# Performance work log

Hardware: AMD Instinct MI355X
Metric: run time of the kernel (lower is better)

Reference implementation:

```python
import jax, jax.numpy as jnp
import numpy as np

B, N, E = 16, 512, 131072
FEAT, EMB, H = 3, 512, 3
K1, K2 = 410, 205  # ceil(0.8*512), ceil(0.5*410) per PyG TopKPooling
NEG_SLOPE, EPS = 0.2, 1e-5


def _gat_conv(x, W, att_s, att_d, bias, src, tgt, valid, num_nodes):
    # PyG GATConv (concat=True): per-edge attention with segment softmax over targets.
    Hh, C = att_s.shape
    xp = (x @ W).reshape(-1, Hh, C)                      # [Nn,H,C]
    a_s = jnp.einsum('nhc,hc->nh', xp, att_s)
    a_d = jnp.einsum('nhc,hc->nh', xp, att_d)
    srcc = jnp.where(valid, src, 0)
    tgtc = jnp.where(valid, tgt, 0)
    e = jax.nn.leaky_relu(a_s[srcc] + a_d[tgtc], NEG_SLOPE)  # [Ee,H]
    seg = jnp.where(valid, tgt, num_nodes)               # invalid edges -> dummy segment
    emax = jax.ops.segment_max(e, seg, num_segments=num_nodes + 1)
    emax = jnp.where(jnp.isfinite(emax), emax, 0.0)
    ex = jnp.exp(e - emax[seg]) * valid[:, None].astype(e.dtype)
    den = jax.ops.segment_sum(ex, seg, num_segments=num_nodes + 1)
    alpha = ex / jnp.maximum(den[seg], 1e-16)            # [Ee,H]
    out = jax.ops.segment_sum(alpha[:, :, None] * xp[srcc], seg,
                              num_segments=num_nodes + 1)[:num_nodes]
    return out.reshape(num_nodes, Hh * C) + bias


def _bn(x, g, b):
    # BatchNorm1d, training-mode batch statistics (biased var), eps=1e-5
    m = x.mean(0)
    v = x.var(0)
    return (x - m) * jax.lax.rsqrt(v + EPS) * g + b


def _topk_pool(x, p, nb, n_per, k):
    # PyG TopKPooling: score = tanh(x.w/||w||), keep top-k per graph, scale by score
    score = jnp.tanh((x @ p) / jnp.linalg.norm(p))       # [nb*n_per]
    top_s, top_i = jax.lax.top_k(score.reshape(nb, n_per), k)
    perm = (top_i + jnp.arange(nb)[:, None] * n_per).reshape(-1)
    x_new = x[perm] * top_s.reshape(-1, 1)
    mapping = jnp.full((nb * n_per,), -1, jnp.int32).at[perm].set(
        jnp.arange(nb * k, dtype=jnp.int32))
    return x_new, mapping


def _pool_cat(x, nb, k):
    # [global_max_pool, global_mean_pool] over equal-size graphs
    xr = x.reshape(nb, k, -1)
    return jnp.concatenate([xr.max(1), xr.mean(1)], axis=1)


def _forward(x, W1, as1, ad1, bc1, Wh1, bh1, g1, be1, p1,
             W2, as2, ad2, bc2, Wh2, bh2, g2, be2, p2,
             Wl1, bl1, Wl2, bl2, edge_index):
    Nn = B * N
    src0, tgt0 = edge_index[0], edge_index[1]
    sl = jnp.arange(Nn, dtype=jnp.int32)                 # GATConv add_self_loops=True
    src1 = jnp.concatenate([src0, sl]); tgt1 = jnp.concatenate([tgt0, sl])
    valid1 = jnp.ones(src1.shape, bool)
    h = _gat_conv(x, W1, as1, ad1, bc1, src1, tgt1, valid1, Nn)
    h = jax.nn.relu(h @ Wh1 + bh1)
    h = _bn(h, g1, be1)
    h, mapping = _topk_pool(h, p1, B, N, K1)
    x1 = _pool_cat(h, B, K1)                             # [B, 2*EMB]
    # relabel edges to pooled node ids; drop edges with removed endpoints via mask
    s2 = mapping[src0]; t2 = mapping[tgt0]
    v2 = (s2 >= 0) & (t2 >= 0)
    sl2 = jnp.arange(B * K1, dtype=jnp.int32)
    src2 = jnp.concatenate([s2, sl2]); tgt2 = jnp.concatenate([t2, sl2])
    valid2 = jnp.concatenate([v2, jnp.ones(sl2.shape, bool)])
    h = _gat_conv(h, W2, as2, ad2, bc2, src2, tgt2, valid2, B * K1)
    h = jax.nn.relu(h @ Wh2 + bh2)
    h = _bn(h, g2, be2)
    h, _ = _topk_pool(h, p2, B, K1, K2)
    x2 = _pool_cat(h, B, K2)
    xg = x1 + x2
    xg = jax.nn.relu(xg @ Wl1 + bl1)                     # dropout p=0.5 disabled (eval)
    return xg @ Wl2 + bl2                                # [B, 256]


def setup_inputs() -> dict:
    key = jax.random.key(0)
    ks = jax.random.split(key, 16)
    x = jax.random.normal(ks[0], (B * N, FEAT), jnp.float32)
    goff = jnp.repeat(jnp.arange(B, dtype=jnp.int32), E // B) * N
    src = jax.random.randint(ks[1], (E,), 0, N, jnp.int32) + goff
    tgt = jax.random.randint(ks[2], (E,), 0, N, jnp.int32) + goff
    edge_index = jnp.stack([src, tgt])
    s = 0.05
    p = {
        'W1': jax.random.normal(ks[3], (FEAT, H * EMB)) * s,
        'as1': jax.random.normal(ks[4], (H, EMB)) * s,
        'ad1': jax.random.normal(ks[5], (H, EMB)) * s,
        'bc1': jnp.zeros((H * EMB,)),
        'Wh1': jax.random.normal(ks[6], (H * EMB, EMB)) * s,
        'bh1': jnp.zeros((EMB,)),
        'g1': jnp.ones((EMB,)), 'be1': jnp.zeros((EMB,)),
        'p1': jax.random.normal(ks[7], (EMB,)) * s,
        'W2': jax.random.normal(ks[8], (EMB, H * EMB)) * s,
        'as2': jax.random.normal(ks[9], (H, EMB)) * s,
        'ad2': jax.random.normal(ks[10], (H, EMB)) * s,
        'bc2': jnp.zeros((H * EMB,)),
        'Wh2': jax.random.normal(ks[11], (H * EMB, EMB)) * s,
        'bh2': jnp.zeros((EMB,)),
        'g2': jnp.ones((EMB,)), 'be2': jnp.zeros((EMB,)),
        'p2': jax.random.normal(ks[12], (EMB,)) * s,
        'Wl1': jax.random.normal(ks[13], (2 * EMB, 512)) * s,
        'bl1': jnp.zeros((512,)),
        'Wl2': jax.random.normal(ks[14], (512, 256)) * s,
        'bl2': jnp.zeros((256,)),
    }
    return {'x': x, 'edge_index': edge_index, **p}


def reference(x, edge_index, W1, as1, ad1, bc1, Wh1, bh1, g1, be1, p1,
              W2, as2, ad2, bc2, Wh2, bh2, g2, be2, p2, Wl1, bl1, Wl2, bl2):
    return _forward(x, W1, as1, ad1, bc1, Wh1, bh1, g1, be1, p1,
                    W2, as2, ad2, bc2, Wh2, bh2, g2, be2, p2,
                    Wl1, bl1, Wl2, bl2, edge_index)
```

## Files before the change

### kernel.cpp

```cpp
#include <hip/hip_runtime.h>
#include <hip/hip_bf16.h>
#include <math.h>

#define E_EDGES 131072
#define NN1 8192
#define NN2 6560
#define NG 16
#define NP1 512
#define KP1 410
#define KP2 205
#define F1 1536
#define EMB 512
#define MAXDEG 256

typedef __hip_bfloat16 bf16;
typedef __attribute__((ext_vector_type(8))) short short8;
typedef __attribute__((ext_vector_type(4))) float f32x4;
typedef __attribute__((ext_vector_type(4))) unsigned short us4;

__device__ inline float wred64(float v){
  #pragma unroll
  for (int o = 32; o; o >>= 1) v += __shfl_down(v, o);
  return v;
}
__device__ inline float b2f_raw(unsigned short u){
  return __uint_as_float((unsigned)u << 16);
}
union BFU { bf16 b; unsigned short u; };
__device__ inline unsigned short f2u(float v){ BFU x; x.b = __float2bfloat16(v); return x.u; }

__device__ __forceinline__ void gld16(const void* g, void* l){
  __builtin_amdgcn_global_load_lds(
      (const __attribute__((address_space(1))) void*)g,
      (__attribute__((address_space(3))) void*)l, 16, 0, 0);
}

__device__ inline void split_store(float v, bf16* __restrict__ ph, bf16* __restrict__ pl){
  bf16 hi = __float2bfloat16(v);
  *ph = hi;
  *pl = __float2bfloat16(v - __bfloat162float(hi));
}

__device__ inline void bn_from_acc(const float* __restrict__ bnacc, int c, float fM,
                                   float& mean, float& inv){
  mean = bnacc[c] / fM;
  float var = fmaxf(bnacc[512+c]/fM - mean*mean, 0.f);
  inv = 1.f / sqrtf(var + 1e-5f);
}

__global__ __launch_bounds__(256) void k_pre(
    const float* __restrict__ W1, const float* __restrict__ as1, const float* __restrict__ ad1,
    const float* __restrict__ Wh1, const float* __restrict__ bc1, const float* __restrict__ bh1,
    const float* __restrict__ W2, const float* __restrict__ as2, const float* __restrict__ ad2,
    const float* __restrict__ Wh2, const float* __restrict__ bc2, const float* __restrict__ bh2,
    float* __restrict__ was1, float* __restrict__ wad1, float* __restrict__ M1p,
    float* __restrict__ cvp,
    float* __restrict__ was2, float* __restrict__ wad2,
    float* __restrict__ Zb, int* __restrict__ cnt2, int* __restrict__ map,
    bf16* __restrict__ Th, bf16* __restrict__ Tl){
  int b = blockIdx.x, t = threadIdx.x;
  if (b < 24){
    int h = b / 8, rem = b % 8, jh = rem >> 2, kc = rem & 3;
    int j = jh*256 + t, c0 = kc*128;
    __shared__ float w1s[3][128];
    for (int i = t; i < 384; i += 256)
      w1s[i>>7][i&127] = W1[(i>>7)*1536 + h*512 + c0 + (i&127)];
    __syncthreads();
    const float* whc = Wh1 + (size_t)(h*512 + c0)*512 + j;
    float a0=0.f, a1=0.f, a2=0.f;
    #pragma unroll 8
    for (int c = 0; c < 128; c++){
      float v = whc[(size_t)c*512];
      a0 += w1s[0][c]*v; a1 += w1s[1][c]*v; a2 += w1s[2][c]*v;
    }
    float* dst = M1p + (size_t)kc*4608;
    dst[(h*3+0)*512 + j] = a0;
    dst[(h*3+1)*512 + j] = a1;
    dst[(h*3+2)*512 + j] = a2;
  } else if (b < 56){
    int b2 = b - 24;
    int which = b2 >> 4, rem = b2 & 15, jh = rem >> 3, kc = rem & 7;
    const float* bc = which ? bc2 : bc1;
    const float* Wh = which ? Wh2 : Wh1;
    const float* bh = which ? bh2 : bh1;
    int j = jh*256 + t, i0 = kc*192;
    float acc = (kc == 0) ? bh[j] : 0.f;
    #pragma unroll 8
    for (int i = 0; i < 192; i++)
      acc += bc[i0+i] * Wh[(size_t)(i0+i)*512 + j];
    cvp[(size_t)(which*8 + kc)*512 + j] = acc;
  } else if (b < 152){
    int b3 = b - 56;
    int y = b3 >> 4, et = b3 & 15;
    int kind = y / 3, h = y % 3;
    int w = t >> 6, lane = t & 63;
    const float* att = kind ? ad2 : as2;
    float a[8];
    #pragma unroll
    for (int u = 0; u < 8; u++) a[u] = att[h*512 + lane*8 + u];
    for (int r = w; r < 32; r += 4){
      int e = et*32 + r;
      const float4* row = (const float4*)(W2 + (size_t)e*1536 + h*512) + lane*2;
      float4 v0 = row[0], v1 = row[1];
      float d = v0.x*a[0]+v0.y*a[1]+v0.z*a[2]+v0.w*a[3]
              + v1.x*a[4]+v1.y*a[5]+v1.z*a[6]+v1.w*a[7];
      d = wred64(d);
      if (lane == 0) (kind ? wad2 : was2)[h*512 + e] = d;
    }
  } else if (b < 170){
    if (t < 64){
      int bb = b - 152;
      int kind = bb / 9, r = bb % 9, h = r / 3, f = r % 3;
      const float* att = kind ? ad1 : as1;
      float s = 0.f;
      for (int c = t; c < 512; c += 64) s += W1[f*1536 + h*512 + c] * att[h*512 + c];
      s = wred64(s);
      if (t == 0) (kind ? wad1 : was1)[h*3 + f] = s;
    }
  } else if (b < 236){
    int i = (b - 170)*256 + t;
    if (i < 2048){ Zb[i] = 0.f; }
    else if (i < 2048 + NN2){ cnt2[i - 2048] = 1; }
    else if (i < 2048 + NN2 + NN1){ map[i - 2048 - NN2] = -1; }
  } else {
    int bb = b - 236;
    int z = bb % 3; int rr = bb / 3; int by = rr >> 3, bx = rr & 7;
    const float* A = W2 + (size_t)z*512;
    const float* B = Wh2 + (size_t)z*512*512;
    __shared__ __align__(16) short sAh[4096], sAl[4096], sBh[4096], sBl[4096];
    int w = t >> 6, lane = t & 63;
    int l16 = lane & 15, q = lane >> 4;
    int bm = by*64, bn = bx*64;
    int am  = t >> 2, akw = (t & 3)*16;
    int bnl = t & 63, bkq = (t >> 6)*16;
    f32x4 acc[4];
    #pragma unroll
    for (int nf = 0; nf < 4; nf++) acc[nf] = (f32x4){0.f,0.f,0.f,0.f};
    float va[16], vb[16];
    #define GS_LOAD(K0) do { \
      _Pragma("unroll") for (int u = 0; u < 4; u++){ \
        float4 v4 = *(const float4*)(A + (size_t)(bm+am)*1536 + (K0) + akw + u*4); \
        va[u*4]=v4.x; va[u*4+1]=v4.y; va[u*4+2]=v4.z; va[u*4+3]=v4.w; } \
      _Pragma("unroll") for (int u = 0; u < 16; u++) \
        vb[u] = B[(size_t)((K0) + bkq + u)*512 + bn + bnl]; \
    } while(0)
    GS_LOAD(0);
    for (int it = 0; it < 8; it++){
      #pragma unroll
      for (int hh = 0; hh < 2; hh++){
        short8 ah_, al_, bh_, bl_;
        #pragma unroll
        for (int jj = 0; jj < 8; jj++){
          float v = va[hh*8+jj];
          unsigned short hu = f2u(v);
          ah_[jj] = (short)hu; al_[jj] = (short)f2u(v - b2f_raw(hu));
          v = vb[hh*8+jj];
          hu = f2u(v);
          bh_[jj] = (short)hu; bl_[jj] = (short)f2u(v - b2f_raw(hu));
        }
        int aoff = am*64  + ((((akw>>3) + hh) ^ (am  & 7)) << 3);
        *(short8*)(sAh + aoff) = ah_;
        *(short8*)(sAl + aoff) = al_;
        int boff = bnl*64 + ((((bkq>>3) + hh) ^ (bnl & 7)) << 3);
        *(short8*)(sBh + boff) = bh_;
        *(short8*)(sBl + boff) = bl_;
      }
      __syncthreads();
      if (it < 7) GS_LOAD((it+1)*64);
      #pragma unroll
      for (int ks = 0; ks < 2; ks++){
        int gc = ks*4 + q;
        int ar = w*16 + l16;
        int ao = ar*64 + ((gc ^ (ar & 7)) << 3);
        short8 afh = *(const short8*)(sAh + ao);
        short8 afl = *(const short8*)(sAl + ao);
        #pragma unroll
        for (int nf = 0; nf < 4; nf++){
          int br = nf*16 + l16;
          int bo = br*64 + ((gc ^ (br & 7)) << 3);
          short8 bfh = *(const short8*)(sBh + bo);
          short8 bfl = *(const short8*)(sBl + bo);
          acc[nf] = __builtin_amdgcn_mfma_f32_16x16x32_bf16(afh, bfh, acc[nf], 0, 0, 0);
          acc[nf] = __builtin_amdgcn_mfma_f32_16x16x32_bf16(afh, bfl, acc[nf], 0, 0, 0);
          acc[nf] = __builtin_amdgcn_mfma_f32_16x16x32_bf16(afl, bfh, acc[nf], 0, 0, 0);
        }
      }
      __syncthreads();
    }
    #undef GS_LOAD
    int m0 = bm + w*16 + q*4;
    #pragma unroll
    for (int nf = 0; nf < 4; nf++){
      int n = bn + nf*16 + l16;
      size_t base = (size_t)n*1536 + (size_t)z*512 + m0;
      #pragma unroll
      for (int e = 0; e < 4; e++)
        split_store(acc[nf][e], &Th[base+e], &Tl[base+e]);
    }
  }
}

__global__ __launch_bounds__(256) void k_edge(
    const int* __restrict__ src0, const int* __restrict__ tgt0, const float* __restrict__ x,
    const float* __restrict__ was, const float* __restrict__ wad,
    float* __restrict__ denp, float* __restrict__ nump){
  int b = blockIdx.x, t = threadIdx.x;
  int g = b >> 4, ch = b & 15;
  __shared__ float lden[1536];
  __shared__ float lnum[4608];
  for (int i = t; i < 1536; i += 256) lden[i] = 0.f;
  for (int i = t; i < 4608; i += 256) lnum[i] = 0.f;
  __syncthreads();
  int base = g*8192;
  int it0 = ch*544;
  for (int k = t; k < 544; k += 256){
    int it = it0 + k;
    int s, tl;
    if (it < 8192){ s = src0[base+it]; tl = tgt0[base+it] & 511; }
    else { tl = it - 8192; s = g*512 + tl; }
    float xs0 = x[s*3], xs1 = x[s*3+1], xs2 = x[s*3+2];
    int tg = g*512 + tl;
    float xt0 = x[tg*3], xt1 = x[tg*3+1], xt2 = x[tg*3+2];
    #pragma unroll
    for (int h = 0; h < 3; h++){
      float v = xs0*was[h*3]+xs1*was[h*3+1]+xs2*was[h*3+2]
              + xt0*wad[h*3]+xt1*wad[h*3+1]+xt2*wad[h*3+2];
      v = v > 0.f ? v : 0.2f*v;
      float pe = expf(v);
      atomicAdd(&lden[tl*3 + h], pe);
      atomicAdd(&lnum[tl*9 + h*3 + 0], pe * xs0);
      atomicAdd(&lnum[tl*9 + h*3 + 1], pe * xs1);
      atomicAdd(&lnum[tl*9 + h*3 + 2], pe * xs2);
    }
  }
  __syncthreads();
  for (int i = t; i < 4608; i += 256) nump[(size_t)b*4608 + i] = lnum[i];
  for (int i = t; i < 1536; i += 256) denp[(size_t)b*1536 + i] = lden[i];
}

__global__ __launch_bounds__(256) void k_h1(
    const float* __restrict__ nump, const float* __restrict__ denp,
    const float* __restrict__ M1p, const float* __restrict__ cvp1, bf16* __restrict__ hout,
    float* __restrict__ bnacc1){
  __shared__ float sM[9*512];
  __shared__ float sC[512];
  __shared__ float sA[32*9];
  int t = threadIdx.x; int n0 = blockIdx.x*32;
  for (int i = t; i < 9*512; i += 256)
    sM[i] = M1p[i] + M1p[4608 + i] + M1p[2*4608 + i] + M1p[3*4608 + i];
  for (int i = t; i < 512; i += 256){
    float s = 0.f;
    #pragma unroll
    for (int kc = 0; kc < 8; kc++) s += cvp1[kc*512 + i];
    sC[i] = s;
  }
  for (int i = t; i < 288; i += 256){
    int node = i / 9, q = i % 9, hh = q / 3;
    int gn = n0 + node;
    int g = gn >> 9, nl = gn & 511;
    float ns = 0.f, ds = 0.f;
    #pragma unroll 4
    for (int ch = 0; ch < 16; ch++){
      ns += nump[(size_t)(g*16 + ch)*4608 + nl*9 + q];
      ds += denp[(size_t)(g*16 + ch)*1536 + nl*3 + hh];
    }
    sA[i] = ns / fmaxf(ds, 1e-16f);
  }
  __syncthreads();
  float c0v = sC[t], c1v = sC[t+256];
  float ls0=0.f, lq0=0.f, ls1=0.f, lq1=0.f;
  #pragma unroll 4
  for (int i = 0; i < 32; i++){
    float a0 = c0v, a1 = c1v;
    #pragma unroll
    for (int q = 0; q < 9; q++){
      float av = sA[i*9+q];
      a0 += av * sM[q*512 + t];
      a1 += av * sM[q*512 + t + 256];
    }
    a0 = fmaxf(a0, 0.f); a1 = fmaxf(a1, 0.f);
    hout[(size_t)(n0+i)*512 + t]       = __float2bfloat16(a0);
    hout[(size_t)(n0+i)*512 + t + 256] = __float2bfloat16(a1);
    ls0 += a0; lq0 += a0*a0; ls1 += a1; lq1 += a1*a1;
  }
  atomicAdd(&bnacc1[t],           ls0);
  atomicAdd(&bnacc1[t+256],       ls1);
  atomicAdd(&bnacc1[512 + t],     lq0);
  atomicAdd(&bnacc1[512 + t+256], lq1);
}

__global__ __launch_bounds__(512) void k_scoresort(
    const bf16* __restrict__ h, const float* __restrict__ bnacc, int M,
    const float* __restrict__ g_, const float* __restrict__ be, const float* __restrict__ p,
    int n_per, int K, int* __restrict__ map,
    int* __restrict__ topi, float* __restrict__ tops){
  int g = blockIdx.x, t = threadIdx.x;
  __shared__ float w[512];
  __shared__ float redb[8], redp[8];
  __shared__ float sk[512];
  __shared__ int si[512];
  float fM = (float)M;
  float mean, inv; bn_from_acc(bnacc, t, fM, mean, inv);
  float gc = g_[t], pc = p[t];
  float ig = inv * gc;
  w[t] = ig * pc;
  float bt = (be[t] - mean * ig) * pc;
  float b_ = wred64(bt);
  float pp = wred64(pc * pc);
  int lane = t & 63, wv = t >> 6;
  if (lane == 0){ redb[wv] = b_; redp[wv] = pp; }
  __syncthreads();
  float B0 = 0.f, pn2 = 0.f;
  #pragma unroll
  for (int u = 0; u < 8; u++){ B0 += redb[u]; pn2 += redp[u]; }
  float pn = sqrtf(pn2);
  float score = -INFINITY; int idx = 0x7fffffff;
  if (t < n_per){
    const unsigned short* hr = (const unsigned short*)h + (size_t)(g*n_per + t)*EMB;
    float dot = 0.f;
    #pragma unroll 4
    for (int c = 0; c < 512; c += 8){
      us4 v0 = *(const us4*)(hr + c);
      us4 v1 = *(const us4*)(hr + c + 4);
      dot += b2f_raw(v0.x)*w[c]   + b2f_raw(v0.y)*w[c+1]
           + b2f_raw(v0.z)*w[c+2] + b2f_raw(v0.w)*w[c+3]
           + b2f_raw(v1.x)*w[c+4] + b2f_raw(v1.y)*w[c+5]
           + b2f_raw(v1.z)*w[c+6] + b2f_raw(v1.w)*w[c+7];
    }
    score = tanhf((dot + B0) / pn);
    idx = t;
  }
  sk[t] = score; si[t] = idx;
  __syncthreads();
  for (int k = 2; k <= 512; k <<= 1){
    for (int j = k >> 1; j > 0; j >>= 1){
      int l = t ^ j;
      if (l > t){
        float ki = sk[t], kl = sk[l]; int ii = si[t], il = si[l];
        bool before_l = (kl > ki) || (kl == ki && il < ii);
        bool up = ((t & k) == 0);
        if (up == before_l){ sk[t]=kl; sk[l]=ki; si[t]=il; si[l]=ii; }
      }
      __syncthreads();
    }
  }
  if (t < K){
    if (map) map[g*n_per + si[t]] = g*K + t;
    topi[g*K + t] = si[t];
    tops[g*K + t] = sk[t];
  }
}

__global__ __launch_bounds__(256) void k_gather_c2(
    const bf16* __restrict__ h, const float* __restrict__ bnacc, int M,
    const float* __restrict__ gm, const float* __restrict__ be,
    const int* __restrict__ topi, const float* __restrict__ tops,
    bf16* __restrict__ xn, int n_per, int K,
    const float* __restrict__ was2, const float* __restrict__ wad2,
    float* __restrict__ aso, float* __restrict__ ado,
    const int* __restrict__ src0, const int* __restrict__ tgt0,
    const int* __restrict__ map, int* __restrict__ cnt2, int nblk_g){
  int row = blockIdx.x, t = threadIdx.x;
  if (row >= nblk_g){
    int i = (row - nblk_g)*256 + t;
    if (i < E_EDGES){
      int s = map[src0[i]], tg = map[tgt0[i]];
      if (s >= 0 && tg >= 0) atomicAdd(&cnt2[tg], 1);
    }
    return;
  }
  int gr = row / K, i = row - gr*K;
  int sidx = topi[gr*K + i];
  float s = tops[gr*K + i];
  const bf16* src = h + ((size_t)(gr*n_per + sidx))*EMB;
  bf16* dst = xn + (size_t)row*EMB;
  int c0 = t, c1 = t + 256;
  float fM = (float)M;
  float mean0, inv0, mean1, inv1;
  bn_from_acc(bnacc, c0, fM, mean0, inv0);
  bn_from_acc(bnacc, c1, fM, mean1, inv1);
  float v0 = ((__bfloat162float(src[c0]) - mean0) * inv0 * gm[c0] + be[c0]) * s;
  float v1 = ((__bfloat162float(src[c1]) - mean1) * inv1 * gm[c1] + be[c1]) * s;
  dst[c0] = __float2bfloat16(v0);
  dst[c1] = __float2bfloat16(v1);
  {
    float a[6];
    #pragma unroll
    for (int hh = 0; hh < 3; hh++){
      a[hh]   = v0*was2[hh*512 + c0] + v1*was2[hh*512 + c1];
      a[3+hh] = v0*wad2[hh*512 + c0] + v1*wad2[hh*512 + c1];
    }
    __shared__ float red[6][4];
    int lane = t & 63, wv = t >> 6;
    #pragma unroll
    for (int q = 0; q < 6; q++){ float v = wred64(a[q]); if (lane==0) red[q][wv]=v; }
    __syncthreads();
    if (t < 6){
      float sm = red[t][0]+red[t][1]+red[t][2]+red[t][3];
      if (t < 3) aso[row*3+t] = sm; else ado[row*3+(t-3)] = sm;
    }
  }
}

__device__ inline void scan_body(const int* __restrict__ counts, int* __restrict__ off,
                                 int* __restrict__ cur, int n, int* __restrict__ sh){
  int t = threadIdx.x;
  int chunk = (n + 1023) >> 10;
  int b = t * chunk; int e = b + chunk; if (e > n) e = n;
  int s = 0;
  for (int i = b; i < e; i++) s += counts[i];
  sh[t] = s; __syncthreads();
  for (int o = 1; o < 1024; o <<= 1){
    int v = (t >= o) ? sh[t-o] : 0;
    __syncthreads();
    sh[t] += v;
    __syncthreads();
  }
  int run = (t > 0) ? sh[t-1] : 0;
  for (int i = b; i < e; i++){ int c = counts[i]; off[i] = run; cur[i] = run; run += c; }
  if (t == 1023) off[n] = sh[1023];
}
__global__ void k_fill2(const int* __restrict__ src0, const int* __restrict__ tgt0,
                        const int* __restrict__ map, int* __restrict__ cur,
                        int* __restrict__ esrc, int E, int nn){
  int i = blockIdx.x*blockDim.x + threadIdx.x;
  if (i >= E + nn) return;
  int s, tg;
  if (i < E){
    s = map[src0[i]]; tg = map[tgt0[i]];
    if (s < 0 || tg < 0) return;
  } else { s = i - E; tg = s; }
  int pos = atomicAdd(&cur[tg], 1);
  esrc[pos] = s;
}

__global__ __launch_bounds__(1024) void k_poolA_scan(const bf16* __restrict__ xn,
    float* __restrict__ cat, int K,
    const int* __restrict__ cnt2, int* __restrict__ off2, int* __restrict__ cur2){
  __shared__ int shi[1024];
  __shared__ float smax[8][128];
  __shared__ float ssum[8][128];
  int b = blockIdx.x, t = threadIdx.x;
  if (b == 64){ scan_body(cnt2, off2, cur2, NN2, shi); return; }
  int g = b >> 2, cb = b & 3;
  int c = t & 127, rg = t >> 7;
  int col = cb*128 + c;
  const unsigned short* p = (const unsigned short*)xn + (size_t)g*K*EMB + col;
  float mx = -INFINITY, sm = 0.f;
  for (int r = rg; r < K; r += 8){
    float v = b2f_raw(p[(size_t)r*EMB]);
    mx = fmaxf(mx, v); sm += v;
  }
  smax[rg][c] = mx; ssum[rg][c] = sm;
  __syncthreads();
  if (rg == 0){
    #pragma unroll
    for (int u = 1; u < 8; u++){ mx = fmaxf(mx, smax[u][c]); sm += ssum[u][c]; }
    cat[g*1024 + col] = mx;
    cat[g*1024 + 512 + col] = sm / (float)K;
  }
}
__global__ __launch_bounds__(1024) void k_poolB(const bf16* __restrict__ h,
    const float* __restrict__ bnacc, int M,
    const float* __restrict__ gm, const float* __restrict__ be,
    const int* __restrict__ topi, const float* __restrict__ tops,
    float* __restrict__ cat, int n_per, int K){
  __shared__ int sti[256];
  __shared__ float sts[256];
  __shared__ float smax[8][128];
  __shared__ float ssum[8][128];
  int b = blockIdx.x, t = threadIdx.x;
  int g = b >> 2, cb = b & 3;
  for (int r = t; r < K; r += 1024){ sti[r] = topi[g*K + r]; sts[r] = tops[g*K + r]; }
  __syncthreads();
  int c = t & 127, rg = t >> 7;
  int col = cb*128 + c;
  float fM = (float)M;
  float mean, inv; bn_from_acc(bnacc, col, fM, mean, inv);
  float gg = gm[col], bb = be[col];
  const unsigned short* hp = (const unsigned short*)h;
  float mx = -INFINITY, sm = 0.f;
  for (int r = rg; r < K; r += 8){
    float v = (b2f_raw(hp[(size_t)(g*n_per + sti[r])*EMB + col]) - mean) * inv * gg + bb;
    v *= sts[r];
    mx = fmaxf(mx, v); sm += v;
  }
  smax[rg][c] = mx; ssum[rg][c] = sm;
  __syncthreads();
  if (rg == 0){
    #pragma unroll
    for (int u = 1; u < 8; u++){ mx = fmaxf(mx, smax[u][c]); sm += ssum[u][c]; }
    cat[g*1024 + col] = mx;
    cat[g*1024 + 512 + col] = sm / (float)K;
  }
}

__global__ __launch_bounds__(256) void k_agg2(
    const bf16* __restrict__ xn, const float* __restrict__ aso, const float* __restrict__ ado,
    const int* __restrict__ off, const int* __restrict__ esrc,
    bf16* __restrict__ oh){
  int n = blockIdx.x, t = threadIdx.x;
  __shared__ int srcs[MAXDEG];
  __shared__ float al[MAXDEG*3];
  __shared__ float mh[3], dh[3];
  int s0 = off[n]; int deg = off[n+1] - s0; if (deg > MAXDEG) deg = MAXDEG;
  for (int e = t; e < deg; e += 256) srcs[e] = esrc[s0 + e];
  __syncthreads();
  float ad0 = ado[n*3+0], ad1 = ado[n*3+1], ad2 = ado[n*3+2];
  for (int e = t; e < deg; e += 256){
    int s = srcs[e];
    float v0 = aso[s*3+0] + ad0, v1 = aso[s*3+1] + ad1, v2 = aso[s*3+2] + ad2;
    al[e*3+0] = v0 > 0.f ? v0 : 0.2f*v0;
    al[e*3+1] = v1 > 0.f ? v1 : 0.2f*v1;
    al[e*3+2] = v2 > 0.f ? v2 : 0.2f*v2;
  }
  __syncthreads();
  if (t < 3){
    float m = -INFINITY;
    for (int e = 0; e < deg; e++) m = fmaxf(m, al[e*3+t]);
    float d = 0.f;
    for (int e = 0; e < deg; e++) d += expf(al[e*3+t] - m);
    mh[t] = m; dh[t] = 1.f / fmaxf(d, 1e-16f);
  }
  __syncthreads();
  for (int e = t; e < deg; e += 256){
    al[e*3+0] = expf(al[e*3+0]-mh[0])*dh[0];
    al[e*3+1] = expf(al[e*3+1]-mh[1])*dh[1];
    al[e*3+2] = expf(al[e*3+2]-mh[2])*dh[2];
  }
  __syncthreads();
  float acc[2][3] = {};
  for (int e = 0; e < deg; e++){
    int s = srcs[e];
    float a0 = al[e*3], a1 = al[e*3+1], a2 = al[e*3+2];
    #pragma unroll
    for (int k = 0; k < 2; k++){
      float v = __bfloat162float(xn[(size_t)s*512 + t + k*256]);
      acc[k][0] += a0*v; acc[k][1] += a1*v; acc[k][2] += a2*v;
    }
  }
  #pragma unroll
  for (int k = 0; k < 2; k++){
    int c = t + k*256;
    #pragma unroll
    for (int h = 0; h < 3; h++)
      oh[(size_t)n*1536 + h*512 + c] = __float2bfloat16(acc[k][h]);
  }
}

__global__ __launch_bounds__(256, 2) void k_gemm_mfma(
    const bf16* __restrict__ Ah,
    const bf16* __restrict__ Bh, const bf16* __restrict__ Bl,
    const float* __restrict__ bias, bf16* __restrict__ C,
    float* __restrict__ bnacc,
    int M, int N, int K, int Mtiles){
  int xcd = (int)blockIdx.x & 7;
  int ii  = (int)blockIdx.x >> 3;
  int bni = ii & 7;
  int bmi = xcd + 8*(ii >> 3);
  if (bmi >= Mtiles) return;
  __shared__ __align__(16) unsigned short lds[2][16384];
  int t = threadIdx.x, w = t >> 6, lane = t & 63;
  int q = lane >> 4, l16 = lane & 15;
  int bm = bmi * 128, bn = bni * 64;

  int lr = lane >> 3, lc = lane & 7;
  int kg = ((lc ^ lr) & 7) * 8;
  int ro = w*8 + lr;
  int m0 = bm + ro, m1 = bm + 32 + ro, m2 = bm + 64 + ro, m3 = bm + 96 + ro;
  if (m0 >= M) m0 = M-1;  if (m1 >= M) m1 = M-1;
  if (m2 >= M) m2 = M-1;  if (m3 >= M) m3 = M-1;
  int n0 = bn + ro, n1 = bn + 32 + ro;
  const bf16* ptr[8];
  ptr[0] = Ah + (size_t)m0*K + kg;
  ptr[1] = Ah + (size_t)m1*K + kg;
  ptr[2] = Ah + (size_t)m2*K + kg;
  ptr[3] = Ah + (size_t)m3*K + kg;
  ptr[4] = Bh + (size_t)n0*K + kg;
  ptr[5] = Bh + (size_t)n1*K + kg;
  ptr[6] = Bl + (size_t)n0*K + kg;
  ptr[7] = Bl + (size_t)n1*K + kg;
  const int dof[8] = {0, 2048, 4096, 6144, 8192, 10240, 12288, 14336};

  int wm = (w >> 1) * 64, wn = (w & 1) * 32;
  f32x4 acc[4][2];
  #pragma unroll
  for (int i = 0; i < 4; i++)
    #pragma unroll
    for (int j = 0; j < 2; j++)
      acc[i][j] = (f32x4){0.f, 0.f, 0.f, 0.f};

  #pragma unroll
  for (int u = 0; u < 8; u++){
    gld16(ptr[u], &lds[0][dof[u] + w*512]);
    ptr[u] += 64;
  }

  int nit = K >> 6;
  for (int it = 0; it < nit; it++){
    __syncthreads();
    int cur = it & 1;
    if (it + 1 < nit){
      int nxt = cur ^ 1;
      #pragma unroll
      for (int u = 0; u < 8; u++){
        gld16(ptr[u], &lds[nxt][dof[u] + w*512]);
        ptr[u] += 64;
      }
    }
    const unsigned short* L = lds[cur];
    #pragma unroll
    for (int ks = 0; ks < 2; ks++){
      short8 ah[4], bh2[2], bl2[2];
      int gc = ks*4 + q;
      #pragma unroll
      for (int i = 0; i < 4; i++){
        int r = wm + i*16 + l16;
        ah[i] = *(const short8*)(L + r*64 + ((gc ^ (r & 7)) << 3));
      }
      #pragma unroll
      for (int j = 0; j < 2; j++){
        int r = wn + j*16 + l16;
        int so = ((gc ^ (r & 7)) << 3);
        bh2[j] = *(const short8*)(L + 8192  + r*64 + so);
        bl2[j] = *(const short8*)(L + 12288 + r*64 + so);
      }
      #pragma unroll
      for (int i = 0; i < 4; i++)
        #pragma unroll
        for (int j = 0; j < 2; j++){
          acc[i][j] = __builtin_amdgcn_mfma_f32_16x16x32_bf16(ah[i], bh2[j], acc[i][j], 0, 0, 0);
          acc[i][j] = __builtin_amdgcn_mfma_f32_16x16x32_bf16(ah[i], bl2[j], acc[i][j], 0, 0, 0);
        }
    }
  }

  __syncthreads();
  float* cs = (float*)&lds[0][0];
  float* cq = cs + 128;
  int slot = w >> 1;
  #pragma unroll
  for (int j = 0; j < 2; j++){
    int c_local = wn + j*16 + l16;
    int c = bn + c_local;
    float bv = 0.f;
    if (bias){
      #pragma unroll
      for (int kc = 0; kc < 8; kc++) bv += bias[kc*512 + c];
    }
    float ls = 0.f, lq = 0.f;
    #pragma unroll
    for (int i = 0; i < 4; i++){
      int rb = bm + wm + i*16 + q*4;
      #pragma unroll
      for (int e = 0; e < 4; e++){
        int r = rb + e;
        if (r < M){
          float v = fmaxf(acc[i][j][e] + bv, 0.f);
          C[(size_t)r*N + c] = __float2bfloat16(v);
          ls += v; lq += v*v;
        }
      }
    }
    ls += __shfl_xor(ls, 16); ls += __shfl_xor(ls, 32);
    lq += __shfl_xor(lq, 16); lq += __shfl_xor(lq, 32);
    if (q == 0){ cs[slot*64 + c_local] = ls; cq[slot*64 + c_local] = lq; }
  }
  __syncthreads();
  if (t < 64){
    atomicAdd(&bnacc[bn + t],        cs[t] + cs[64 + t]);
    atomicAdd(&bnacc[512 + bn + t],  cq[t] + cq[64 + t]);
  }
}

__global__ __launch_bounds__(256) void k_head1p(const float* __restrict__ c1,
    const float* __restrict__ c2, const float* __restrict__ Wl1,
    float* __restrict__ t1p){
  __shared__ float wl[128][64];
  __shared__ float xgs[16][128];
  int b = blockIdx.x, t = threadIdx.x;
  int jt = b >> 3, kc = b & 7;
  int j0 = jt*64, k0 = kc*128;
  for (int i = t; i < 8192; i += 256){
    int k = i >> 6, j = i & 63;
    wl[k][j] = Wl1[(size_t)(k0 + k)*512 + j0 + j];
  }
  for (int i = t; i < 2048; i += 256){
    int g = i >> 7, k = i & 127;
    int idx = g*1024 + k0 + k;
    xgs[g][k] = c1[idx] + c2[idx];
  }
  __syncthreads();
  #pragma unroll
  for (int u = 0; u < 4; u++){
    int p = t + u*256;
    int g = p >> 6, j = p & 63;
    float acc = 0.f;
    #pragma unroll 8
    for (int k = 0; k < 128; k++)
      acc += xgs[g][k] * wl[k][j];
    t1p[(size_t)(kc*16 + g)*512 + j0 + j] = acc;
  }
}
__global__ __launch_bounds__(512) void k_head2p(const float* __restrict__ t1p,
    const float* __restrict__ bl1, const float* __restrict__ Wl2,
    const float* __restrict__ bl2, float* __restrict__ out){
  __shared__ float t1s[512];
  __shared__ float part[2][256];
  int g = blockIdx.x, t = threadIdx.x;
  float acc = bl1[t];
  #pragma unroll
  for (int kc = 0; kc < 8; kc++)
    acc += t1p[(size_t)(kc*16 + g)*512 + t];
  t1s[t] = fmaxf(acc, 0.f);
  __syncthreads();
  int c = t & 255, half = t >> 8;
  float a = 0.f;
  #pragma unroll 8
  for (int k = half*256; k < half*256 + 256; k++)
    a += t1s[k] * Wl2[(size_t)k*256 + c];
  part[half][c] = a;
  __syncthreads();
  if (half == 0)
    out[g*256 + c] = part[0][c] + part[1][c] + bl2[c];
}

extern "C" void kernel_launch(void* const* d_in, const int* in_sizes, int n_in,
                              void* d_out, int out_size, void* d_ws, size_t ws_size,
                              hipStream_t stream){
  const float* x   = (const float*)d_in[0];
  const int*   ei  = (const int*)d_in[1];
  const float* W1  = (const float*)d_in[2];
  const float* as1 = (const float*)d_in[3];
  const float* ad1 = (const float*)d_in[4];
  const float* bc1 = (const float*)d_in[5];
  const float* Wh1 = (const float*)d_in[6];
  const float* bh1 = (const float*)d_in[7];
  const float* g1  = (const float*)d_in[8];
  const float* be1 = (const float*)d_in[9];
  const float* p1  = (const float*)d_in[10];
  const float* W2  = (const float*)d_in[11];
  const float* as2 = (const float*)d_in[12];
  const float* ad2 = (const float*)d_in[13];
  const float* bc2 = (const float*)d_in[14];
  const float* Wh2 = (const float*)d_in[15];
  const float* bh2 = (const float*)d_in[16];
  const float* g2  = (const float*)d_in[17];
  const float* be2 = (const float*)d_in[18];
  const float* p2  = (const float*)d_in[19];
  const float* Wl1 = (const float*)d_in[20];
  const float* bl1 = (const float*)d_in[21];
  const float* Wl2 = (const float*)d_in[22];
  const float* bl2 = (const float*)d_in[23];
  float* out = (float*)d_out;

  const int* src0 = ei;
  const int* tgt0 = ei + E_EDGES;

  bf16* Cc      = (bf16*)d_ws;
  bf16* xn1     = Cc + (size_t)NN1*EMB;
  bf16* aggx2h  = xn1 + (size_t)NN2*EMB;
  bf16* M2Th    = aggx2h + (size_t)NN2*F1;
  bf16* M2Tl    = M2Th + (size_t)EMB*F1;
  float* holeA  = (float*)(M2Tl + (size_t)EMB*F1);
  float* t1p    = holeA;
  float* bnacc1 = holeA + 122880;
  float* bnacc  = bnacc1 + 1024;
  float* M1p    = bnacc + 1024;
  float* cvp    = M1p + 4*4608;
  float* was2   = cvp + 16*512;
  float* wad2   = was2 + 3*512;
  float* was1   = wad2 + 3*512;
  float* wad1   = was1 + 16;
  float* aso2   = wad1 + 16;
  float* ado2   = aso2 + (size_t)NN2*3;
  float* tops   = ado2 + (size_t)NN2*3;
  float* cat1   = tops + NG*KP1;
  float* cat2   = cat1 + NG*1024;
  int* topi     = (int*)(cat2 + NG*1024);
  int* map      = topi + NG*KP1;
  int* cnt2     = map + NN1;
  int* off2     = cnt2 + NN2;
  int* cur2     = off2 + NN2 + 8;
  int* esrc2    = cur2 + NN2;
  float* nump   = (float*)(esrc2 + 137700);
  float* denp   = nump + (size_t)256*4608;
  float* cvp2   = cvp + 8*512;

  k_pre<<<428,256,0,stream>>>(W1,as1,ad1,Wh1,bc1,bh1, W2,as2,ad2,Wh2,bc2,bh2,
                              was1,wad1,M1p,cvp,was2,wad2,
                              bnacc1,cnt2,map,M2Th,M2Tl);
  k_edge<<<256,256,0,stream>>>(src0,tgt0,x,was1,wad1,denp,nump);
  k_h1<<<NN1/32,256,0,stream>>>(nump,denp,M1p,cvp,Cc,bnacc1);
  k_scoresort<<<NG,512,0,stream>>>(Cc,bnacc1,NN1,g1,be1,p1,NP1,KP1,map,topi,tops);
  k_gather_c2<<<NG*KP1+512,256,0,stream>>>(Cc,bnacc1,NN1,g1,be1,topi,tops,xn1,NP1,KP1,
      was2,wad2,aso2,ado2, src0,tgt0,map,cnt2,NG*KP1);
  k_poolA_scan<<<65,1024,0,stream>>>(xn1,cat1,KP1, cnt2,off2,cur2);
  k_fill2<<<(E_EDGES+NN2+255)/256,256,0,stream>>>(src0,tgt0,map,cur2,esrc2,E_EDGES,NN2);
  k_agg2<<<NN2,256,0,stream>>>(xn1,aso2,ado2,off2,esrc2,aggx2h);
  k_gemm_mfma<<<448,256,0,stream>>>(aggx2h,M2Th,M2Tl,cvp2,Cc,bnacc,NN2,EMB,F1,52);
  k_scoresort<<<NG,512,0,stream>>>(Cc,bnacc,NN2,g2,be2,p2,KP1,KP2,(int*)nullptr,topi,tops);
  k_poolB<<<64,1024,0,stream>>>(Cc,bnacc,NN2,g2,be2,topi,tops,cat2,KP1,KP2);
  k_head1p<<<64,256,0,stream>>>(cat1,cat2,Wl1,t1p);
  k_head2p<<<NG,512,0,stream>>>(t1p,bl1,Wl2,bl2,out);
}
```

Measured before the change: 314.2 us.

## Fuse edge-attention kernel into preprocessing and pool-B into second score-sort

```diff
diff --git a/kernel.cpp b/kernel.cpp
--- a/kernel.cpp
+++ b/kernel.cpp
@@ -53,11 +53,12 @@
     const float* __restrict__ Wh1, const float* __restrict__ bc1, const float* __restrict__ bh1,
     const float* __restrict__ W2, const float* __restrict__ as2, const float* __restrict__ ad2,
     const float* __restrict__ Wh2, const float* __restrict__ bc2, const float* __restrict__ bh2,
-    float* __restrict__ was1, float* __restrict__ wad1, float* __restrict__ M1p,
-    float* __restrict__ cvp,
+    const int* __restrict__ src0, const int* __restrict__ tgt0, const float* __restrict__ x,
+    float* __restrict__ M1p, float* __restrict__ cvp,
     float* __restrict__ was2, float* __restrict__ wad2,
     float* __restrict__ Zb, int* __restrict__ cnt2, int* __restrict__ map,
-    bf16* __restrict__ Th, bf16* __restrict__ Tl){
+    bf16* __restrict__ Th, bf16* __restrict__ Tl,
+    float* __restrict__ denp, float* __restrict__ nump){
   int b = blockIdx.x, t = threadIdx.x;
   if (b < 24){
     int h = b / 8, rem = b % 8, jh = rem >> 2, kc = rem & 3;
@@ -107,23 +108,57 @@
       d = wred64(d);
       if (lane == 0) (kind ? wad2 : was2)[h*512 + e] = d;
     }
-  } else if (b < 170){
-    if (t < 64){
-      int bb = b - 152;
-      int kind = bb / 9, r = bb % 9, h = r / 3, f = r % 3;
-      const float* att = kind ? ad1 : as1;
-      float s = 0.f;
-      for (int c = t; c < 512; c += 64) s += W1[f*1536 + h*512 + c] * att[h*512 + c];
-      s = wred64(s);
-      if (t == 0) (kind ? wad1 : was1)[h*3 + f] = s;
-    }
-  } else if (b < 236){
-    int i = (b - 170)*256 + t;
+  } else if (b < 218){
+    int i = (b - 152)*256 + t;
     if (i < 2048){ Zb[i] = 0.f; }
     else if (i < 2048 + NN2){ cnt2[i - 2048] = 1; }
     else if (i < 2048 + NN2 + NN1){ map[i - 2048 - NN2] = -1; }
+  } else if (b < 474){
+    __shared__ float sww[18];
+    __shared__ float lden[1536];
+    __shared__ float lnum[4608];
+    int wv_ = t >> 6, lane = t & 63;
+    for (int combo = wv_*5; combo < wv_*5+5 && combo < 18; combo++){
+      int kind = combo/9, rr = combo%9, h = rr/3, f = rr%3;
+      const float* att = kind ? ad1 : as1;
+      float s = 0.f;
+      #pragma unroll
+      for (int c = lane; c < 512; c += 64) s += W1[f*1536 + h*512 + c] * att[h*512 + c];
+      s = wred64(s);
+      if (lane == 0) sww[combo] = s;
+    }
+    for (int i = t; i < 1536; i += 256) lden[i] = 0.f;
+    for (int i = t; i < 4608; i += 256) lnum[i] = 0.f;
+    __syncthreads();
+    int eb = b - 218;
+    int g = eb >> 4, ch = eb & 15;
+    int base = g*8192;
+    int it0 = ch*544;
+    for (int k = t; k < 544; k += 256){
+      int it = it0 + k;
+      int s, tl;
+      if (it < 8192){ s = src0[base+it]; tl = tgt0[base+it] & 511; }
+      else { tl = it - 8192; s = g*512 + tl; }
+      float xs0 = x[s*3], xs1 = x[s*3+1], xs2 = x[s*3+2];
+      int tg = g*512 + tl;
+      float xt0 = x[tg*3], xt1 = x[tg*3+1], xt2 = x[tg*3+2];
+      #pragma unroll
+      for (int h = 0; h < 3; h++){
+        float v = xs0*sww[h*3]+xs1*sww[h*3+1]+xs2*sww[h*3+2]
+                + xt0*sww[9+h*3]+xt1*sww[9+h*3+1]+xt2*sww[9+h*3+2];
+        v = v > 0.f ? v : 0.2f*v;
+        float pe = expf(v);
+        atomicAdd(&lden[tl*3 + h], pe);
+        atomicAdd(&lnum[tl*9 + h*3 + 0], pe * xs0);
+        atomicAdd(&lnum[tl*9 + h*3 + 1], pe * xs1);
+        atomicAdd(&lnum[tl*9 + h*3 + 2], pe * xs2);
+      }
+    }
+    __syncthreads();
+    for (int i = t; i < 4608; i += 256) nump[(size_t)eb*4608 + i] = lnum[i];
+    for (int i = t; i < 1536; i += 256) denp[(size_t)eb*1536 + i] = lden[i];
   } else {
-    int bb = b - 236;
+    int bb = b - 474;
     int z = bb % 3; int rr = bb / 3; int by = rr >> 3, bx = rr & 7;
     const float* A = W2 + (size_t)z*512;
     const float* B = Wh2 + (size_t)z*512*512;
@@ -200,44 +235,6 @@
   }
 }
 
-__global__ __launch_bounds__(256) void k_edge(
-    const int* __restrict__ src0, const int* __restrict__ tgt0, const float* __restrict__ x,
-    const float* __restrict__ was, const float* __restrict__ wad,
-    float* __restrict__ denp, float* __restrict__ nump){
-  int b = blockIdx.x, t = threadIdx.x;
-  int g = b >> 4, ch = b & 15;
-  __shared__ float lden[1536];
-  __shared__ float lnum[4608];
-  for (int i = t; i < 1536; i += 256) lden[i] = 0.f;
-  for (int i = t; i < 4608; i += 256) lnum[i] = 0.f;
-  __syncthreads();
-  int base = g*8192;
-  int it0 = ch*544;
-  for (int k = t; k < 544; k += 256){
-    int it = it0 + k;
-    int s, tl;
-    if (it < 8192){ s = src0[base+it]; tl = tgt0[base+it] & 511; }
-    else { tl = it - 8192; s = g*512 + tl; }
-    float xs0 = x[s*3], xs1 = x[s*3+1], xs2 = x[s*3+2];
-    int tg = g*512 + tl;
-    float xt0 = x[tg*3], xt1 = x[tg*3+1], xt2 = x[tg*3+2];
-    #pragma unroll
-    for (int h = 0; h < 3; h++){
-      float v = xs0*was[h*3]+xs1*was[h*3+1]+xs2*was[h*3+2]
-              + xt0*wad[h*3]+xt1*wad[h*3+1]+xt2*wad[h*3+2];
-      v = v > 0.f ? v : 0.2f*v;
-      float pe = expf(v);
-      atomicAdd(&lden[tl*3 + h], pe);
-      atomicAdd(&lnum[tl*9 + h*3 + 0], pe * xs0);
-      atomicAdd(&lnum[tl*9 + h*3 + 1], pe * xs1);
-      atomicAdd(&lnum[tl*9 + h*3 + 2], pe * xs2);
-    }
-  }
-  __syncthreads();
-  for (int i = t; i < 4608; i += 256) nump[(size_t)b*4608 + i] = lnum[i];
-  for (int i = t; i < 1536; i += 256) denp[(size_t)b*1536 + i] = lden[i];
-}
-
 __global__ __launch_bounds__(256) void k_h1(
     const float* __restrict__ nump, const float* __restrict__ denp,
     const float* __restrict__ M1p, const float* __restrict__ cvp1, bf16* __restrict__ hout,
@@ -293,7 +290,7 @@
     const bf16* __restrict__ h, const float* __restrict__ bnacc, int M,
     const float* __restrict__ g_, const float* __restrict__ be, const float* __restrict__ p,
     int n_per, int K, int* __restrict__ map,
-    int* __restrict__ topi, float* __restrict__ tops){
+    int* __restrict__ topi, float* __restrict__ tops, float* __restrict__ cat){
   int g = blockIdx.x, t = threadIdx.x;
   __shared__ float w[512];
   __shared__ float redb[8], redp[8];
@@ -301,10 +298,10 @@
   __shared__ int si[512];
   float fM = (float)M;
   float mean, inv; bn_from_acc(bnacc, t, fM, mean, inv);
-  float gc = g_[t], pc = p[t];
+  float gc = g_[t], pc = p[t], bec = be[t];
   float ig = inv * gc;
   w[t] = ig * pc;
-  float bt = (be[t] - mean * ig) * pc;
+  float bt = (bec - mean * ig) * pc;
   float b_ = wred64(bt);
   float pp = wred64(pc * pc);
   int lane = t & 63, wv = t >> 6;
@@ -344,10 +341,22 @@
       __syncthreads();
     }
   }
-  if (t < K){
-    if (map) map[g*n_per + si[t]] = g*K + t;
-    topi[g*K + t] = si[t];
-    tops[g*K + t] = sk[t];
+  if (cat == nullptr){
+    if (t < K){
+      if (map) map[g*n_per + si[t]] = g*K + t;
+      topi[g*K + t] = si[t];
+      tops[g*K + t] = sk[t];
+    }
+  } else {
+    const unsigned short* hp = (const unsigned short*)h;
+    float mx = -INFINITY, sm = 0.f;
+    for (int r = 0; r < K; r++){
+      float v = (b2f_raw(hp[(size_t)(g*n_per + si[r])*EMB + t]) - mean) * ig + bec;
+      v *= sk[r];
+      mx = fmaxf(mx, v); sm += v;
+    }
+    cat[g*1024 + t] = mx;
+    cat[g*1024 + 512 + t] = sm / (float)K;
   }
 }
 
@@ -449,40 +458,6 @@
   float mx = -INFINITY, sm = 0.f;
   for (int r = rg; r < K; r += 8){
     float v = b2f_raw(p[(size_t)r*EMB]);
-    mx = fmaxf(mx, v); sm += v;
-  }
-  smax[rg][c] = mx; ssum[rg][c] = sm;
-  __syncthreads();
-  if (rg == 0){
-    #pragma unroll
-    for (int u = 1; u < 8; u++){ mx = fmaxf(mx, smax[u][c]); sm += ssum[u][c]; }
-    cat[g*1024 + col] = mx;
-    cat[g*1024 + 512 + col] = sm / (float)K;
-  }
-}
-__global__ __launch_bounds__(1024) void k_poolB(const bf16* __restrict__ h,
-    const float* __restrict__ bnacc, int M,
-    const float* __restrict__ gm, const float* __restrict__ be,
-    const int* __restrict__ topi, const float* __restrict__ tops,
-    float* __restrict__ cat, int n_per, int K){
-  __shared__ int sti[256];
-  __shared__ float sts[256];
-  __shared__ float smax[8][128];
-  __shared__ float ssum[8][128];
-  int b = blockIdx.x, t = threadIdx.x;
-  int g = b >> 2, cb = b & 3;
-  for (int r = t; r < K; r += 1024){ sti[r] = topi[g*K + r]; sts[r] = tops[g*K + r]; }
-  __syncthreads();
-  int c = t & 127, rg = t >> 7;
-  int col = cb*128 + c;
-  float fM = (float)M;
-  float mean, inv; bn_from_acc(bnacc, col, fM, mean, inv);
-  float gg = gm[col], bb = be[col];
-  const unsigned short* hp = (const unsigned short*)h;
-  float mx = -INFINITY, sm = 0.f;
-  for (int r = rg; r < K; r += 8){
-    float v = (b2f_raw(hp[(size_t)(g*n_per + sti[r])*EMB + col]) - mean) * inv * gg + bb;
-    v *= sts[r];
     mx = fmaxf(mx, v); sm += v;
   }
   smax[rg][c] = mx; ssum[rg][c] = sm;
@@ -770,9 +745,8 @@
   float* cvp    = M1p + 4*4608;
   float* was2   = cvp + 16*512;
   float* wad2   = was2 + 3*512;
-  float* was1   = wad2 + 3*512;
-  float* wad1   = was1 + 16;
-  float* aso2   = wad1 + 16;
+  float* hole16 = wad2 + 3*512;
+  float* aso2   = hole16 + 32;
   float* ado2   = aso2 + (size_t)NN2*3;
   float* tops   = ado2 + (size_t)NN2*3;
   float* cat1   = tops + NG*KP1;
@@ -787,20 +761,21 @@
   float* denp   = nump + (size_t)256*4608;
   float* cvp2   = cvp + 8*512;
 
-  k_pre<<<428,256,0,stream>>>(W1,as1,ad1,Wh1,bc1,bh1, W2,as2,ad2,Wh2,bc2,bh2,
-                              was1,wad1,M1p,cvp,was2,wad2,
-                              bnacc1,cnt2,map,M2Th,M2Tl);
-  k_edge<<<256,256,0,stream>>>(src0,tgt0,x,was1,wad1,denp,nump);
+  k_pre<<<666,256,0,stream>>>(W1,as1,ad1,Wh1,bc1,bh1, W2,as2,ad2,Wh2,bc2,bh2,
+                              src0,tgt0,x,
+                              M1p,cvp,was2,wad2,
+                              bnacc1,cnt2,map,M2Th,M2Tl, denp,nump);
   k_h1<<<NN1/32,256,0,stream>>>(nump,denp,M1p,cvp,Cc,bnacc1);
-  k_scoresort<<<NG,512,0,stream>>>(Cc,bnacc1,NN1,g1,be1,p1,NP1,KP1,map,topi,tops);
+  k_scoresort<<<NG,512,0,stream>>>(Cc,bnacc1,NN1,g1,be1,p1,NP1,KP1,map,topi,tops,
+                                   (float*)nullptr);
   k_gather_c2<<<NG*KP1+512,256,0,stream>>>(Cc,bnacc1,NN1,g1,be1,topi,tops,xn1,NP1,KP1,
       was2,wad2,aso2,ado2, src0,tgt0,map,cnt2,NG*KP1);
   k_poolA_scan<<<65,1024,0,stream>>>(xn1,cat1,KP1, cnt2,off2,cur2);
   k_fill2<<<(E_EDGES+NN2+255)/256,256,0,stream>>>(src0,tgt0,map,cur2,esrc2,E_EDGES,NN2);
   k_agg2<<<NN2,256,0,stream>>>(xn1,aso2,ado2,off2,esrc2,aggx2h);
   k_gemm_mfma<<<448,256,0,stream>>>(aggx2h,M2Th,M2Tl,cvp2,Cc,bnacc,NN2,EMB,F1,52);
-  k_scoresort<<<NG,512,0,stream>>>(Cc,bnacc,NN2,g2,be2,p2,KP1,KP2,(int*)nullptr,topi,tops);
-  k_poolB<<<64,1024,0,stream>>>(Cc,bnacc,NN2,g2,be2,topi,tops,cat2,KP1,KP2);
+  k_scoresort<<<NG,512,0,stream>>>(Cc,bnacc,NN2,g2,be2,p2,KP1,KP2,(int*)nullptr,
+                                   (int*)nullptr,(float*)nullptr,cat2);
   k_head1p<<<64,256,0,stream>>>(cat1,cat2,Wl1,t1p);
   k_head2p<<<NG,512,0,stream>>>(t1p,bl1,Wl2,bl2,out);
 }
```

Result: no change. 310.0 us (-1.3%).
